# Kernel tuning notes

Hardware: AMD Instinct MI355X
Metric: run time of the kernel (lower is better)

## Reference

```python
import jax, jax.numpy as jnp
import numpy as np

B, SQ, SK = 2, 2048, 2048
D, H = 1024, 16
HD = D // H              # head_dim = 64
R = 128                  # rel_pos_max_distance
P = 2 * R + 1            # num_pos_ids = 257
RADIUS = 256             # local_attention_radius


def setup_inputs() -> dict:
    key = jax.random.key(0)
    ks = jax.random.split(key, 8)
    s = 0.02
    return {
        "Q": jax.random.normal(ks[0], (B, SQ, D), dtype=jnp.float32),
        "K": jax.random.normal(ks[1], (B, SK, D), dtype=jnp.float32),
        "V": jax.random.normal(ks[2], (B, SK, D), dtype=jnp.float32),
        "Wq": jax.random.normal(ks[3], (D, D), dtype=jnp.float32) * s,
        "Wk": jax.random.normal(ks[4], (D, D), dtype=jnp.float32) * s,
        "Wv": jax.random.normal(ks[5], (D, D), dtype=jnp.float32) * s,
        "Wo": jax.random.normal(ks[6], (D, D), dtype=jnp.float32) * s,
        "E": jax.random.normal(ks[7], (P, D), dtype=jnp.float32) * s,  # rel_embeds
    }


def _split_heads(x, W):
    # bias-free projection then split: B x S x D -> B x H x S x HD
    y = x @ W.T
    b, s, _ = y.shape
    return y.reshape(b, s, H, HD).transpose(0, 2, 1, 3)


def reference(Q, K, V, Wq, Wk, Wv, Wo, E):
    q = _split_heads(Q, Wq)  # B,H,Sq,HD
    k = _split_heads(K, Wk)  # B,H,Sk,HD
    v = _split_heads(V, Wv)  # B,H,Sk,HD

    # rel_embeds reshape matches torch: E[p] viewed as (head_dim, num_heads)
    rel = E.reshape(P, HD, H).transpose(2, 0, 1)           # H,P,HD
    Q_rel = jnp.einsum("bhqd,hpd->bhqp", q, rel)           # B,H,Sq,P

    # slided relative position ids: clip(j - i, -R, R) + R
    i = jnp.arange(SQ)[:, None]
    j = jnp.arange(SK)[None, :]
    rel_ids = jnp.clip(j - i, -R, R) + R                   # Sq,Sk
    rel_shift = jnp.take_along_axis(
        Q_rel, jnp.broadcast_to(rel_ids, (B, H, SQ, SK)), axis=3
    )                                                       # B,H,Sq,Sk

    energy = (jnp.einsum("bhqd,bhkd->bhqk", q, k) + rel_shift) / jnp.sqrt(
        jnp.float32(HD)
    )

    # local attention mask: True = masked (outside window of radius RADIUS)
    mask = jnp.abs(j - i) > RADIUS                          # Sq,Sk
    mask = mask & ~jnp.all(mask, axis=-1, keepdims=True)    # never mask full rows
    energy = jnp.where(mask[None, None], -jnp.inf, energy)

    attn = jax.nn.softmax(energy, axis=-1)                  # B,H,Sq,Sk
    out = jnp.einsum("bhqk,bhkd->bhqd", attn, v)            # B,H,Sq,HD
    # torch: view(B,H,Sq,HD).permute(0,2,3,1).flatten(2,3) -> B,Sq,(HD*H)
    out = out.transpose(0, 2, 3, 1).reshape(B, SQ, D)
    return out @ Wo.T
```

## Files before the change

### kernel.cpp

```cpp
#include <hip/hip_runtime.h>
#include <hip/hip_bf16.h>

#define BATCH 2
#define SQn 2048
#define SKn 2048
#define DMODEL 1024
#define NH 16
#define HD 64
#define NPOS 257
#define RWIN 128
#define RADIUS 256

typedef __attribute__((ext_vector_type(8))) short bf16x8;
typedef __attribute__((ext_vector_type(4))) float f32x4;

static __device__ __forceinline__ unsigned short f2bf(float f) {
    union { float f; unsigned u; } v; v.f = f;
    unsigned r = (v.u + 0x7FFFu + ((v.u >> 16) & 1u)) >> 16;
    return (unsigned short)r;
}
static __device__ __forceinline__ float bf2f(unsigned short b) {
    union { unsigned u; float f; } v; v.u = ((unsigned)b) << 16;
    return v.f;
}

static __device__ __forceinline__ void gl_lds16(const unsigned short* g, unsigned short* l) {
    __builtin_amdgcn_global_load_lds(
        (const __attribute__((address_space(1))) unsigned*)g,
        (__attribute__((address_space(3))) unsigned*)l, 16, 0, 0);
}

#define SWZ(row) (((row) ^ ((row) >> 2)) & 3)

__global__ __launch_bounds__(256) void convert_kernel(
    const float* __restrict__ Q, const float* __restrict__ K, const float* __restrict__ V,
    const float* __restrict__ Wq, const float* __restrict__ Wk, const float* __restrict__ Wv,
    const float* __restrict__ Wo,
    unsigned short* __restrict__ xb,
    unsigned short* __restrict__ wb,
    unsigned short* __restrict__ woh)
{
    int i = blockIdx.x * 256 + threadIdx.x;
    if (i < 3145728) {
        int which = i >> 20;
        int off = i & 1048575;
        const float* src = which == 0 ? Q : (which == 1 ? K : V);
        unsigned short* dst = xb + (size_t)which * 4194304;
        float4 v4 = ((const float4*)src)[off];
        ushort4 o4;
        o4.x = f2bf(v4.x); o4.y = f2bf(v4.y); o4.z = f2bf(v4.z); o4.w = f2bf(v4.w);
        ((ushort4*)dst)[off] = o4;
    } else {
        int i2 = i - 3145728;
        int which = i2 >> 18;
        int off = i2 & 262143;
        if (which < 3) {
            const float* src = which == 0 ? Wq : (which == 1 ? Wk : Wv);
            unsigned short* dst = wb + (size_t)which * 1048576;
            float4 v4 = ((const float4*)src)[off];
            ushort4 o4;
            o4.x = f2bf(v4.x); o4.y = f2bf(v4.y); o4.z = f2bf(v4.z); o4.w = f2bf(v4.w);
            ((ushort4*)dst)[off] = o4;
        } else {
            float4 v4 = ((const float4*)Wo)[off];
            int e0 = off * 4;
            int n  = e0 >> 10;
            int c0 = e0 & 1023;
            int d  = c0 >> 4;
            int h0 = c0 & 15;
            woh[((size_t)(h0 + 0) * 1024 + n) * 64 + d] = f2bf(v4.x);
            woh[((size_t)(h0 + 1) * 1024 + n) * 64 + d] = f2bf(v4.y);
            woh[((size_t)(h0 + 2) * 1024 + n) * 64 + d] = f2bf(v4.z);
            woh[((size_t)(h0 + 3) * 1024 + n) * 64 + d] = f2bf(v4.w);
        }
    }
}

__global__ __launch_bounds__(256) void mfma_gemm(
    const unsigned short* __restrict__ Xall,
    const unsigned short* __restrict__ Wall,
    unsigned short* __restrict__ Yall)
{
    __shared__ unsigned short sA[128 * 64];
    __shared__ unsigned short sB[128 * 64];
    __shared__ unsigned short sT[64 * 136];

    const int tid  = threadIdx.x;
    const int wv   = tid >> 6;
    const int lane = tid & 63;
    const int quad = lane >> 4;
    const int l15  = lane & 15;
    const int z    = blockIdx.z;
    const int m0   = blockIdx.x * 128;
    const int n0   = blockIdx.y * 128;
    const int wr   = (wv >> 1) * 64;
    const int wc   = (wv & 1) * 64;

    const unsigned short* X = Xall + (size_t)z * (4096 * 1024);
    const unsigned short* W = Wall + (size_t)z * (1024 * 1024);

    int srow[4], scc[4];
#pragma unroll
    for (int it = 0; it < 4; ++it) {
        int f = it * 256 + tid;
        srow[it] = f >> 3;
        scc[it]  = ((f & 7) ^ (srow[it] & 7)) * 8;
    }

    int aoff[2][4], boff[2][4];
#pragma unroll
    for (int ks = 0; ks < 2; ++ks)
#pragma unroll
        for (int t = 0; t < 4; ++t) {
            int R = wr + t * 16 + l15;
            aoff[ks][t] = R * 64 + ((((ks << 2) + quad) ^ (R & 7)) * 8);
            int C = wc + t * 16 + l15;
            boff[ks][t] = C * 64 + ((((ks << 2) + quad) ^ (C & 7)) * 8);
        }

    f32x4 acc[4][4];
#pragma unroll
    for (int i = 0; i < 4; ++i)
#pragma unroll
        for (int j = 0; j < 4; ++j)
            acc[i][j] = (f32x4){0.f, 0.f, 0.f, 0.f};

#pragma unroll
    for (int it = 0; it < 4; ++it) {
        gl_lds16(X + (size_t)(m0 + srow[it]) * 1024 + scc[it], &sA[(it * 256 + tid) * 8]);
        gl_lds16(W + (size_t)(n0 + srow[it]) * 1024 + scc[it], &sB[(it * 256 + tid) * 8]);
    }

    for (int k0 = 0; k0 < 1024; k0 += 64) {
        __syncthreads();

        bf16x8 a0[4], b0[4];
#pragma unroll
        for (int t = 0; t < 4; ++t) a0[t] = *(const bf16x8*)&sA[aoff[0][t]];
#pragma unroll
        for (int t = 0; t < 4; ++t) b0[t] = *(const bf16x8*)&sB[boff[0][t]];
#pragma unroll
        for (int i = 0; i < 4; ++i)
#pragma unroll
            for (int j = 0; j < 4; ++j)
                acc[i][j] = __builtin_amdgcn_mfma_f32_16x16x32_bf16(a0[i], b0[j], acc[i][j], 0, 0, 0);

        bf16x8 a1[4], b1[4];
#pragma unroll
        for (int t = 0; t < 4; ++t) a1[t] = *(const bf16x8*)&sA[aoff[1][t]];
#pragma unroll
        for (int t = 0; t < 4; ++t) b1[t] = *(const bf16x8*)&sB[boff[1][t]];
        __syncthreads();

        if (k0 + 64 < 1024) {
            const int kn = k0 + 64;
#pragma unroll
            for (int it = 0; it < 4; ++it) {
                gl_lds16(X + (size_t)(m0 + srow[it]) * 1024 + kn + scc[it], &sA[(it * 256 + tid) * 8]);
                gl_lds16(W + (size_t)(n0 + srow[it]) * 1024 + kn + scc[it], &sB[(it * 256 + tid) * 8]);
            }
        }
#pragma unroll
        for (int i = 0; i < 4; ++i)
#pragma unroll
            for (int j = 0; j < 4; ++j)
                acc[i][j] = __builtin_amdgcn_mfma_f32_16x16x32_bf16(a1[i], b1[j], acc[i][j], 0, 0, 0);
    }

    unsigned short* Y = Yall + (size_t)z * (4096 * 1024);
    const int b_ = m0 >> 11;
    const int s0 = m0 & (SQn - 1);

    if (z < 2) {
#pragma unroll
        for (int i = 0; i < 4; ++i) {
            int mbase = s0 + wr + i * 16 + quad * 4;
#pragma unroll
            for (int j = 0; j < 4; ++j) {
                int col = n0 + wc + j * 16 + l15;
                int h = col >> 6, dd = col & 63;
                unsigned short* yb = Y + (((size_t)(b_ * NH + h) * SQn) << 6) + dd;
#pragma unroll
                for (int r = 0; r < 4; ++r)
                    yb[(size_t)(mbase + r) << 6] = f2bf(acc[i][j][r]);
            }
        }
    } else {
#pragma unroll
        for (int hh = 0; hh < 2; ++hh) {
            __syncthreads();
            if ((wv & 1) == hh) {
#pragma unroll
                for (int i = 0; i < 4; ++i) {
                    int mloc = wr + i * 16 + quad * 4;
#pragma unroll
                    for (int j = 0; j < 4; ++j) {
                        ushort4 pk;
                        pk.x = f2bf(acc[i][j][0]);
                        pk.y = f2bf(acc[i][j][1]);
                        pk.z = f2bf(acc[i][j][2]);
                        pk.w = f2bf(acc[i][j][3]);
                        *(ushort4*)&sT[(j * 16 + l15) * 136 + mloc] = pk;
                    }
                }
            }
            __syncthreads();
            int h = (n0 >> 6) + hh;
            unsigned short* yb = Y + ((size_t)(b_ * NH + h) * HD) * SKn + s0;
#pragma unroll
            for (int it = 0; it < 4; ++it) {
                int u = it * 256 + tid;
                int dd = u >> 4, mc = u & 15;
                uint4 val = *(const uint4*)&sT[dd * 136 + mc * 8];
                *(uint4*)(yb + (size_t)dd * SKn + mc * 8) = val;
            }
        }
    }
}

__global__ __launch_bounds__(256) void gemm_out(
    const unsigned short* __restrict__ aoh,
    const unsigned short* __restrict__ woh,
    float* __restrict__ Y)
{
    __shared__ unsigned short sA[64 * 64];
    __shared__ unsigned short sB[128 * 64];

    const int tid  = threadIdx.x;
    const int wv   = tid >> 6;
    const int lane = tid & 63;
    const int quad = lane >> 4;
    const int l15  = lane & 15;
    const int m0   = blockIdx.x * 64;
    const int n0   = blockIdx.y * 128;
    const int wr   = (wv >> 1) * 32;
    const int wc   = (wv & 1) * 64;
    const int b_   = m0 >> 11;
    const int s0   = m0 & (SQn - 1);

    int rowa[2], ca[2];
#pragma unroll
    for (int it = 0; it < 2; ++it) {
        int f = it * 256 + tid;
        rowa[it] = f >> 3;
        ca[it]   = ((f & 7) ^ (rowa[it] & 7)) * 8;
    }
    int rowb[4], cb[4];
#pragma unroll
    for (int it = 0; it < 4; ++it) {
        int f = it * 256 + tid;
        rowb[it] = f >> 3;
        cb[it]   = ((f & 7) ^ (rowb[it] & 7)) * 8;
    }

    int aoff[2][2], boff[2][4];
#pragma unroll
    for (int ks = 0; ks < 2; ++ks) {
#pragma unroll
        for (int i = 0; i < 2; ++i) {
            int R = wr + i * 16 + l15;
            aoff[ks][i] = R * 64 + ((((ks << 2) + quad) ^ (R & 7)) * 8);
        }
#pragma unroll
        for (int j = 0; j < 4; ++j) {
            int C = wc + j * 16 + l15;
            boff[ks][j] = C * 64 + ((((ks << 2) + quad) ^ (C & 7)) * 8);
        }
    }

    f32x4 acc[2][4];
#pragma unroll
    for (int i = 0; i < 2; ++i)
#pragma unroll
        for (int j = 0; j < 4; ++j)
            acc[i][j] = (f32x4){0.f, 0.f, 0.f, 0.f};

    {
        const unsigned short* Ah = aoh + ((size_t)(b_ * NH) * SQn + s0) * HD;
        const unsigned short* Bh = woh + (size_t)n0 * HD;
#pragma unroll
        for (int it = 0; it < 2; ++it)
            gl_lds16(Ah + (size_t)rowa[it] * HD + ca[it], &sA[(it * 256 + tid) * 8]);
#pragma unroll
        for (int it = 0; it < 4; ++it)
            gl_lds16(Bh + (size_t)rowb[it] * HD + cb[it], &sB[(it * 256 + tid) * 8]);
    }

    for (int h = 0; h < NH; ++h) {
        __syncthreads();

        bf16x8 a0[2], b0[4];
#pragma unroll
        for (int i = 0; i < 2; ++i) a0[i] = *(const bf16x8*)&sA[aoff[0][i]];
#pragma unroll
        for (int j = 0; j < 4; ++j) b0[j] = *(const bf16x8*)&sB[boff[0][j]];
#pragma unroll
        for (int i = 0; i < 2; ++i)
#pragma unroll
            for (int j = 0; j < 4; ++j)
                acc[i][j] = __builtin_amdgcn_mfma_f32_16x16x32_bf16(a0[i], b0[j], acc[i][j], 0, 0, 0);

        bf16x8 a1[2], b1[4];
#pragma unroll
        for (int i = 0; i < 2; ++i) a1[i] = *(const bf16x8*)&sA[aoff[1][i]];
#pragma unroll
        for (int j = 0; j < 4; ++j) b1[j] = *(const bf16x8*)&sB[boff[1][j]];
        __syncthreads();

        if (h + 1 < NH) {
            const unsigned short* Ah = aoh + ((size_t)(b_ * NH + h + 1) * SQn + s0) * HD;
            const unsigned short* Bh = woh + ((size_t)(h + 1) * 1024 + n0) * HD;
#pragma unroll
            for (int it = 0; it < 2; ++it)
                gl_lds16(Ah + (size_t)rowa[it] * HD + ca[it], &sA[(it * 256 + tid) * 8]);
#pragma unroll
            for (int it = 0; it < 4; ++it)
                gl_lds16(Bh + (size_t)rowb[it] * HD + cb[it], &sB[(it * 256 + tid) * 8]);
        }
#pragma unroll
        for (int i = 0; i < 2; ++i)
#pragma unroll
            for (int j = 0; j < 4; ++j)
                acc[i][j] = __builtin_amdgcn_mfma_f32_16x16x32_bf16(a1[i], b1[j], acc[i][j], 0, 0, 0);
    }

#pragma unroll
    for (int i = 0; i < 2; ++i) {
        int mbase = m0 + wr + i * 16 + quad * 4;
#pragma unroll
        for (int j = 0; j < 4; ++j) {
            int col = n0 + wc + j * 16 + l15;
#pragma unroll
            for (int r = 0; r < 4; ++r)
                Y[(size_t)(mbase + r) * DMODEL + col] = acc[i][j][r];
        }
    }
}

__global__ __launch_bounds__(256) void relt_kernel(
    const float* __restrict__ E, unsigned short* __restrict__ relTb)
{
    int idx = blockIdx.x * 256 + threadIdx.x;
    const int total = NH * NPOS * HD;
    if (idx < total) {
        int d = idx & (HD - 1);
        int p = (idx >> 6) % NPOS;
        int h = idx / (NPOS * HD);
        relTb[idx] = f2bf(E[(size_t)p * DMODEL + d * NH + h]);
    }
}

#define BIAS_S2 0.0014089565402528222f
#define SC2     0.1803368801111204f

__global__ __launch_bounds__(256, 2) void attn_mfma(
    const unsigned short* __restrict__ q,
    const unsigned short* __restrict__ k,
    const unsigned short* __restrict__ vT,
    const unsigned short* __restrict__ relTb,
    unsigned short* __restrict__ aoh)
{
    __shared__ unsigned short sK[64 * 64];
    __shared__ unsigned short sVt[64 * 64];
    __shared__ unsigned short sP[4][16 * 72];
    __shared__ signed char    sq8[128 * 260];
    unsigned short* const sQ = (unsigned short*)sq8;

    const int tid  = threadIdx.x;
    const int w    = tid >> 6;
    const int lane = tid & 63;
    const int quad = lane >> 4;
    const int l15  = lane & 15;
    const int xcd  = blockIdx.x & 7;
    const int sidx = blockIdx.x >> 3;
    const int bh   = (xcd << 2) | (sidx >> 4);
    const int q0   = (sidx & 15) << 7;
    const int h    = bh & (NH - 1);

    const int f1 = tid,       row1 = f1 >> 3;
    const int c1 = ((f1 & 7) ^ (row1 & 7)) * 8;
    const int f2 = 256 + tid, row2 = f2 >> 3;
    const int c2 = ((f2 & 7) ^ (row2 & 7)) * 8;

    {
        const unsigned short* gq = q + ((size_t)bh * SQn + q0) * HD;
#pragma unroll
        for (int it = 0; it < 4; ++it) {
            int f = it * 256 + tid;
            int row = f >> 3;
            int c = ((f & 7) ^ (row & 7)) * 8;
            gl_lds16(gq + row * HD + c, &sQ[f * 8]);
        }
    }
    __syncthreads();

    const int qrow = w * 16 + l15;
    const int qs = (quad ^ (qrow & 7)) * 8;
    bf16x8 a0A = *(const bf16x8*)&sQ[qrow * 64 + qs];
    bf16x8 a1A = *(const bf16x8*)&sQ[qrow * 64 + (qs ^ 32)];
    bf16x8 a0B = *(const bf16x8*)&sQ[(64 + qrow) * 64 + qs];
    bf16x8 a1B = *(const bf16x8*)&sQ[(64 + qrow) * 64 + (qs ^ 32)];

    const int myrow = w * 16 + quad * 4;
    for (int c5 = 0; c5 < 5; ++c5) {
        __syncthreads();
        const unsigned short* gr = relTb + ((size_t)h * NPOS + c5 * 64) * HD;
        gl_lds16(gr + row1 * HD + c1, &sK[f1 * 8]);
        gl_lds16(gr + row2 * HD + c2, &sK[f2 * 8]);
        __syncthreads();
#pragma unroll
        for (int t = 0; t < 4; ++t) {
            int prow = t * 16 + l15;
            int ks = (quad ^ (prow & 7)) * 8;
            bf16x8 b0 = *(const bf16x8*)&sK[prow * 64 + ks];
            bf16x8 b1 = *(const bf16x8*)&sK[prow * 64 + (ks ^ 32)];
            f32x4 ccA = {0.f, 0.f, 0.f, 0.f};
            ccA = __builtin_amdgcn_mfma_f32_16x16x32_bf16(a0A, b0, ccA, 0, 0, 0);
            ccA = __builtin_amdgcn_mfma_f32_16x16x32_bf16(a1A, b1, ccA, 0, 0, 0);
            f32x4 ccB = {0.f, 0.f, 0.f, 0.f};
            ccB = __builtin_amdgcn_mfma_f32_16x16x32_bf16(a0B, b0, ccB, 0, 0, 0);
            ccB = __builtin_amdgcn_mfma_f32_16x16x32_bf16(a1B, b1, ccB, 0, 0, 0);
            int pos = c5 * 64 + t * 16 + l15;
            if (pos < NPOS) {
#pragma unroll
                for (int r = 0; r < 4; ++r) {
                    int iqA = (int)rintf(ccA[r] * 128.0f);
                    iqA = iqA < -127 ? -127 : (iqA > 127 ? 127 : iqA);
                    sq8[(myrow + r) * 260 + pos] = (signed char)iqA;
                    int iqB = (int)rintf(ccB[r] * 128.0f);
                    iqB = iqB < -127 ? -127 : (iqB > 127 ? 127 : iqB);
                    sq8[(64 + myrow + r) * 260 + pos] = (signed char)iqB;
                }
            }
        }
    }
    __syncthreads();

    float bias0A[4], bias256A[4], bias0B[4], bias256B[4];
#pragma unroll
    for (int r = 0; r < 4; ++r) {
        bias0A[r]   = (float)sq8[(myrow + r) * 260 + 0]          * BIAS_S2;
        bias256A[r] = (float)sq8[(myrow + r) * 260 + 256]        * BIAS_S2;
        bias0B[r]   = (float)sq8[(64 + myrow + r) * 260 + 0]     * BIAS_S2;
        bias256B[r] = (float)sq8[(64 + myrow + r) * 260 + 256]   * BIAS_S2;
    }

    const int lo = (q0 - RADIUS) > 0 ? (q0 - RADIUS) : 0;
    const int hi = (q0 + 127 + RADIUS) < (SKn - 1) ? (q0 + 127 + RADIUS) : (SKn - 1);
    const int nt = ((hi - lo) >> 6) + 1;
    const int e_ = l15 - quad * 4;

    const unsigned short* kg = k  + (size_t)bh * SKn * HD;
    const unsigned short* vg = vT + (size_t)bh * HD * SKn;

    float laccA[4] = {0.f, 0.f, 0.f, 0.f};
    float laccB[4] = {0.f, 0.f, 0.f, 0.f};
    f32x4 oA[4], oB[4];
#pragma unroll
    for (int t = 0; t < 4; ++t) {
        oA[t] = (f32x4){0.f, 0.f, 0.f, 0.f};
        oB[t] = (f32x4){0.f, 0.f, 0.f, 0.f};
    }

    {
        gl_lds16(kg + (size_t)(lo + row1) * HD + c1, &sK[f1 * 8]);
        gl_lds16(kg + (size_t)(lo + row2) * HD + c2, &sK[f2 * 8]);
        gl_lds16(vg + (size_t)row1 * SKn + lo + c1, &sVt[f1 * 8]);
        gl_lds16(vg + (size_t)row2 * SKn + lo + c2, &sVt[f2 * 8]);
    }

    for (int kt = 0; kt < nt; ++kt) {
        const int kb = lo + (kt << 6);
        __syncthreads();

        bf16x8 kf0[4], kf1[4], vf0[4], vf1[4];
#pragma unroll
        for (int t = 0; t < 4; ++t) {
            int prow = t * 16 + l15;
            int ks = (quad ^ (prow & 7)) * 8;
            kf0[t] = *(const bf16x8*)&sK[prow * 64 + ks];
            kf1[t] = *(const bf16x8*)&sK[prow * 64 + (ks ^ 32)];
            vf0[t] = *(const bf16x8*)&sVt[prow * 64 + ks];
            vf1[t] = *(const bf16x8*)&sVt[prow * 64 + (ks ^ 32)];
        }
        __syncthreads();

        if (kt + 1 < nt) {
            const int kb2 = kb + 64;
            gl_lds16(kg + (size_t)(kb2 + row1) * HD + c1, &sK[f1 * 8]);
            gl_lds16(kg + (size_t)(kb2 + row2) * HD + c2, &sK[f2 * 8]);
            gl_lds16(vg + (size_t)row1 * SKn + kb2 + c1, &sVt[f1 * 8]);
            gl_lds16(vg + (size_t)row2 * SKn + kb2 + c2, &sVt[f2 * 8]);
        }

        const int dtbaseA = kb - q0 - w * 16;
        if (dtbaseA > -320 && dtbaseA < 272) {
#pragma unroll
            for (int t = 0; t < 4; ++t) {
                const int dt = dtbaseA + t * 16;
                const int spb = (quad * 4) * 72 + t * 16 + l15;
                if (dt <= -272 || dt >= 272) {
#pragma unroll
                    for (int r = 0; r < 4; ++r) sP[w][spb + r * 72] = 0;
                } else {
                    f32x4 sc = {0.f, 0.f, 0.f, 0.f};
                    sc = __builtin_amdgcn_mfma_f32_16x16x32_bf16(a0A, kf0[t], sc, 0, 0, 0);
                    sc = __builtin_amdgcn_mfma_f32_16x16x32_bf16(a1A, kf1[t], sc, 0, 0, 0);

                    float pv[4];
                    if (dt >= -112 && dt <= 112) {
                        int idx0 = myrow * 260 + dt + 128 + e_;
#pragma unroll
                        for (int r = 0; r < 4; ++r) {
                            float bf = (float)sq8[idx0 + r * 259] * BIAS_S2;
                            pv[r] = __builtin_amdgcn_exp2f(fmaf(sc[r], SC2, bf));
                        }
                    } else if (dt >= -240 && dt <= -144) {
#pragma unroll
                        for (int r = 0; r < 4; ++r)
                            pv[r] = __builtin_amdgcn_exp2f(fmaf(sc[r], SC2, bias0A[r]));
                    } else if (dt >= 144 && dt <= 240) {
#pragma unroll
                        for (int r = 0; r < 4; ++r)
                            pv[r] = __builtin_amdgcn_exp2f(fmaf(sc[r], SC2, bias256A[r]));
                    } else {
#pragma unroll
                        for (int r = 0; r < 4; ++r) {
                            int d = dt + e_ - r;
                            bool in = (unsigned)(d + RADIUS) <= 2u * RADIUS;
                            int p = d < -RWIN ? 0 : (d > RWIN ? 2 * RWIN : d + RWIN);
                            float bf = (float)sq8[(myrow + r) * 260 + p] * BIAS_S2;
                            float e = __builtin_amdgcn_exp2f(fmaf(sc[r], SC2, bf));
                            pv[r] = in ? e : 0.0f;
                        }
                    }
#pragma unroll
                    for (int r = 0; r < 4; ++r) {
                        unsigned short pb = f2bf(pv[r]);
                        sP[w][spb + r * 72] = pb;
                        laccA[r] += bf2f(pb);
                    }
                }
            }
            bf16x8 p0 = *(const bf16x8*)&sP[w][l15 * 72 + quad * 8];
            bf16x8 p1 = *(const bf16x8*)&sP[w][l15 * 72 + 32 + quad * 8];
#pragma unroll
            for (int t = 0; t < 4; ++t) {
                oA[t] = __builtin_amdgcn_mfma_f32_16x16x32_bf16(p0, vf0[t], oA[t], 0, 0, 0);
                oA[t] = __builtin_amdgcn_mfma_f32_16x16x32_bf16(p1, vf1[t], oA[t], 0, 0, 0);
            }
        }

        const int dtbaseB = dtbaseA - 64;
        if (dtbaseB > -320 && dtbaseB < 272) {
#pragma unroll
            for (int t = 0; t < 4; ++t) {
                const int dt = dtbaseB + t * 16;
                const int spb = (quad * 4) * 72 + t * 16 + l15;
                if (dt <= -272 || dt >= 272) {
#pragma unroll
                    for (int r = 0; r < 4; ++r) sP[w][spb + r * 72] = 0;
                } else {
                    f32x4 sc = {0.f, 0.f, 0.f, 0.f};
                    sc = __builtin_amdgcn_mfma_f32_16x16x32_bf16(a0B, kf0[t], sc, 0, 0, 0);
                    sc = __builtin_amdgcn_mfma_f32_16x16x32_bf16(a1B, kf1[t], sc, 0, 0, 0);

                    float pv[4];
                    if (dt >= -112 && dt <= 112) {
                        int idx0 = (64 + myrow) * 260 + dt + 128 + e_;
#pragma unroll
                        for (int r = 0; r < 4; ++r) {
                            float bf = (float)sq8[idx0 + r * 259] * BIAS_S2;
                            pv[r] = __builtin_amdgcn_exp2f(fmaf(sc[r], SC2, bf));
                        }
                    } else if (dt >= -240 && dt <= -144) {
#pragma unroll
                        for (int r = 0; r < 4; ++r)
                            pv[r] = __builtin_amdgcn_exp2f(fmaf(sc[r], SC2, bias0B[r]));
                    } else if (dt >= 144 && dt <= 240) {
#pragma unroll
                        for (int r = 0; r < 4; ++r)
                            pv[r] = __builtin_amdgcn_exp2f(fmaf(sc[r], SC2, bias256B[r]));
                    } else {
#pragma unroll
                        for (int r = 0; r < 4; ++r) {
                            int d = dt + e_ - r;
                            bool in = (unsigned)(d + RADIUS) <= 2u * RADIUS;
                            int p = d < -RWIN ? 0 : (d > RWIN ? 2 * RWIN : d + RWIN);
                            float bf = (float)sq8[(64 + myrow + r) * 260 + p] * BIAS_S2;
                            float e = __builtin_amdgcn_exp2f(fmaf(sc[r], SC2, bf));
                            pv[r] = in ? e : 0.0f;
                        }
                    }
#pragma unroll
                    for (int r = 0; r < 4; ++r) {
                        unsigned short pb = f2bf(pv[r]);
                        sP[w][spb + r * 72] = pb;
                        laccB[r] += bf2f(pb);
                    }
                }
            }
            bf16x8 p0 = *(const bf16x8*)&sP[w][l15 * 72 + quad * 8];
            bf16x8 p1 = *(const bf16x8*)&sP[w][l15 * 72 + 32 + quad * 8];
#pragma unroll
            for (int t = 0; t < 4; ++t) {
                oB[t] = __builtin_amdgcn_mfma_f32_16x16x32_bf16(p0, vf0[t], oB[t], 0, 0, 0);
                oB[t] = __builtin_amdgcn_mfma_f32_16x16x32_bf16(p1, vf1[t], oB[t], 0, 0, 0);
            }
        }
    }

    float linvA[4], linvB[4];
#pragma unroll
    for (int r = 0; r < 4; ++r) {
        float lA = laccA[r];
        float lB = laccB[r];
#pragma unroll
        for (int off = 1; off <= 8; off <<= 1) {
            lA += __shfl_xor(lA, off);
            lB += __shfl_xor(lB, off);
        }
        linvA[r] = 1.0f / lA;
        linvB[r] = 1.0f / lB;
    }

    unsigned short* ob = aoh + ((size_t)bh * SQn + q0) * HD;
#pragma unroll
    for (int t = 0; t < 4; ++t) {
#pragma unroll
        for (int r = 0; r < 4; ++r) {
            int irow = w * 16 + quad * 4 + r;
            ob[irow * HD + t * 16 + l15] = f2bf(oA[t][r] * linvA[r]);
            ob[(64 + irow) * HD + t * 16 + l15] = f2bf(oB[t][r] * linvB[r]);
        }
    }
}

extern "C" void kernel_launch(void* const* d_in, const int* in_sizes, int n_in,
                              void* d_out, int out_size, void* d_ws, size_t ws_size,
                              hipStream_t stream) {
    const float* Q  = (const float*)d_in[0];
    const float* K  = (const float*)d_in[1];
    const float* V  = (const float*)d_in[2];
    const float* Wq = (const float*)d_in[3];
    const float* Wk = (const float*)d_in[4];
    const float* Wv = (const float*)d_in[5];
    const float* Wo = (const float*)d_in[6];
    const float* E  = (const float*)d_in[7];
    float* out = (float*)d_out;

    char* p = (char*)d_ws;
    unsigned short* xb    = (unsigned short*)p; p += (size_t)24 << 20;
    unsigned short* wb    = (unsigned short*)p; p += (size_t)6  << 20;
    unsigned short* woh   = (unsigned short*)p; p += (size_t)2  << 20;
    unsigned short* head  = (unsigned short*)p; p += (size_t)24 << 20;
    unsigned short* relTb = (unsigned short*)p; p += (size_t)1  << 20;
    unsigned short* aoh   = (unsigned short*)p;

    unsigned short* qb  = head;
    unsigned short* kb  = head + 4194304;
    unsigned short* vTb = head + 8388608;

    dim3 bb(256);
    convert_kernel<<<dim3(16384), bb, 0, stream>>>(Q, K, V, Wq, Wk, Wv, Wo, xb, wb, woh);
    relt_kernel<<<dim3(1028), bb, 0, stream>>>(E, relTb);
    mfma_gemm<<<dim3(32, 8, 3), bb, 0, stream>>>(xb, wb, head);
    attn_mfma<<<dim3(BATCH * NH * (SQn / 128)), bb, 0, stream>>>(qb, kb, vTb, relTb, aoh);
    gemm_out<<<dim3(64, 8), bb, 0, stream>>>(aoh, woh, out);
}
```

Measured before the change: 205.0 us.

## Double-buffer LDS tiles in projection and output GEMMs

The projection GEMM moves to a K-step of 32 with two LDS buffers and a new swizzle, so the next tile's global-to-LDS load is issued before computing on the current one, with a single barrier per step. The output GEMM also gets ping-pong LDS buffers for its per-head A and B tiles and drops its second barrier. This is meant to overlap global loads with MFMA work and cut synchronisation. The cost is more LDS per block in gemm_out, which may lower occupancy, and twice as many loop iterations in the projection GEMM.

```diff
diff --git a/kernel.cpp b/kernel.cpp
--- a/kernel.cpp
+++ b/kernel.cpp
@@ -29,8 +29,6 @@
         (const __attribute__((address_space(1))) unsigned*)g,
         (__attribute__((address_space(3))) unsigned*)l, 16, 0, 0);
 }
-
-#define SWZ(row) (((row) ^ ((row) >> 2)) & 3)
 
 __global__ __launch_bounds__(256) void convert_kernel(
     const float* __restrict__ Q, const float* __restrict__ K, const float* __restrict__ V,
@@ -81,9 +79,7 @@
     const unsigned short* __restrict__ Wall,
     unsigned short* __restrict__ Yall)
 {
-    __shared__ unsigned short sA[128 * 64];
-    __shared__ unsigned short sB[128 * 64];
-    __shared__ unsigned short sT[64 * 136];
+    __shared__ unsigned short S[16384];
 
     const int tid  = threadIdx.x;
     const int wv   = tid >> 6;
@@ -99,24 +95,22 @@
     const unsigned short* X = Xall + (size_t)z * (4096 * 1024);
     const unsigned short* W = Wall + (size_t)z * (1024 * 1024);
 
-    int srow[4], scc[4];
-#pragma unroll
-    for (int it = 0; it < 4; ++it) {
+    int srow[2], scol[2];
+#pragma unroll
+    for (int it = 0; it < 2; ++it) {
         int f = it * 256 + tid;
-        srow[it] = f >> 3;
-        scc[it]  = ((f & 7) ^ (srow[it] & 7)) * 8;
-    }
-
-    int aoff[2][4], boff[2][4];
-#pragma unroll
-    for (int ks = 0; ks < 2; ++ks)
-#pragma unroll
-        for (int t = 0; t < 4; ++t) {
-            int R = wr + t * 16 + l15;
-            aoff[ks][t] = R * 64 + ((((ks << 2) + quad) ^ (R & 7)) * 8);
-            int C = wc + t * 16 + l15;
-            boff[ks][t] = C * 64 + ((((ks << 2) + quad) ^ (C & 7)) * 8);
-        }
+        srow[it] = f >> 2;
+        scol[it] = ((f & 3) ^ ((srow[it] >> 1) & 3)) * 8;
+    }
+
+    int aoff[4], boff[4];
+#pragma unroll
+    for (int t = 0; t < 4; ++t) {
+        int R = wr + t * 16 + l15;
+        aoff[t] = R * 32 + ((quad ^ ((R >> 1) & 3)) * 8);
+        int C = wc + t * 16 + l15;
+        boff[t] = C * 32 + ((quad ^ ((C >> 1) & 3)) * 8);
+    }
 
     f32x4 acc[4][4];
 #pragma unroll
@@ -126,45 +120,41 @@
             acc[i][j] = (f32x4){0.f, 0.f, 0.f, 0.f};
 
 #pragma unroll
-    for (int it = 0; it < 4; ++it) {
-        gl_lds16(X + (size_t)(m0 + srow[it]) * 1024 + scc[it], &sA[(it * 256 + tid) * 8]);
-        gl_lds16(W + (size_t)(n0 + srow[it]) * 1024 + scc[it], &sB[(it * 256 + tid) * 8]);
-    }
-
-    for (int k0 = 0; k0 < 1024; k0 += 64) {
+    for (int it = 0; it < 2; ++it) {
+        int f = it * 256 + tid;
+        gl_lds16(X + (size_t)(m0 + srow[it]) * 1024 + scol[it], &S[f * 8]);
+        gl_lds16(W + (size_t)(n0 + srow[it]) * 1024 + scol[it], &S[8192 + f * 8]);
+    }
+
+    for (int k0 = 0; k0 < 1024; k0 += 32) {
+        const int cur = (k0 >> 5) & 1;
         __syncthreads();
 
-        bf16x8 a0[4], b0[4];
-#pragma unroll
-        for (int t = 0; t < 4; ++t) a0[t] = *(const bf16x8*)&sA[aoff[0][t]];
-#pragma unroll
-        for (int t = 0; t < 4; ++t) b0[t] = *(const bf16x8*)&sB[boff[0][t]];
+        if (k0 + 32 < 1024) {
+            const int nxt = cur ^ 1;
+            const int kn = k0 + 32;
+#pragma unroll
+            for (int it = 0; it < 2; ++it) {
+                int f = it * 256 + tid;
+                gl_lds16(X + (size_t)(m0 + srow[it]) * 1024 + kn + scol[it],
+                         &S[nxt * 4096 + f * 8]);
+                gl_lds16(W + (size_t)(n0 + srow[it]) * 1024 + kn + scol[it],
+                         &S[8192 + nxt * 4096 + f * 8]);
+            }
+        }
+
+        const unsigned short* bA = &S[cur * 4096];
+        const unsigned short* bB = &S[8192 + cur * 4096];
+        bf16x8 a[4], b[4];
+#pragma unroll
+        for (int t = 0; t < 4; ++t) a[t] = *(const bf16x8*)&bA[aoff[t]];
+#pragma unroll
+        for (int t = 0; t < 4; ++t) b[t] = *(const bf16x8*)&bB[boff[t]];
 #pragma unroll
         for (int i = 0; i < 4; ++i)
 #pragma unroll
             for (int j = 0; j < 4; ++j)
-                acc[i][j] = __builtin_amdgcn_mfma_f32_16x16x32_bf16(a0[i], b0[j], acc[i][j], 0, 0, 0);
-
-        bf16x8 a1[4], b1[4];
-#pragma unroll
-        for (int t = 0; t < 4; ++t) a1[t] = *(const bf16x8*)&sA[aoff[1][t]];
-#pragma unroll
-        for (int t = 0; t < 4; ++t) b1[t] = *(const bf16x8*)&sB[boff[1][t]];
-        __syncthreads();
-
-        if (k0 + 64 < 1024) {
-            const int kn = k0 + 64;
-#pragma unroll
-            for (int it = 0; it < 4; ++it) {
-                gl_lds16(X + (size_t)(m0 + srow[it]) * 1024 + kn + scc[it], &sA[(it * 256 + tid) * 8]);
-                gl_lds16(W + (size_t)(n0 + srow[it]) * 1024 + kn + scc[it], &sB[(it * 256 + tid) * 8]);
-            }
-        }
-#pragma unroll
-        for (int i = 0; i < 4; ++i)
-#pragma unroll
-            for (int j = 0; j < 4; ++j)
-                acc[i][j] = __builtin_amdgcn_mfma_f32_16x16x32_bf16(a1[i], b1[j], acc[i][j], 0, 0, 0);
+                acc[i][j] = __builtin_amdgcn_mfma_f32_16x16x32_bf16(a[i], b[j], acc[i][j], 0, 0, 0);
     }
 
     unsigned short* Y = Yall + (size_t)z * (4096 * 1024);
@@ -186,6 +176,7 @@
             }
         }
     } else {
+        unsigned short* const sT = S;
 #pragma unroll
         for (int hh = 0; hh < 2; ++hh) {
             __syncthreads();
@@ -223,8 +214,7 @@
     const unsigned short* __restrict__ woh,
     float* __restrict__ Y)
 {
-    __shared__ unsigned short sA[64 * 64];
-    __shared__ unsigned short sB[128 * 64];
+    __shared__ unsigned short S[24576];
 
     const int tid  = threadIdx.x;
     const int wv   = tid >> 6;
@@ -280,20 +270,38 @@
         const unsigned short* Bh = woh + (size_t)n0 * HD;
 #pragma unroll
         for (int it = 0; it < 2; ++it)
-            gl_lds16(Ah + (size_t)rowa[it] * HD + ca[it], &sA[(it * 256 + tid) * 8]);
+            gl_lds16(Ah + (size_t)rowa[it] * HD + ca[it], &S[(it * 256 + tid) * 8]);
 #pragma unroll
         for (int it = 0; it < 4; ++it)
-            gl_lds16(Bh + (size_t)rowb[it] * HD + cb[it], &sB[(it * 256 + tid) * 8]);
+            gl_lds16(Bh + (size_t)rowb[it] * HD + cb[it], &S[8192 + (it * 256 + tid) * 8]);
     }
 
     for (int h = 0; h < NH; ++h) {
+        const int cur = h & 1;
         __syncthreads();
 
+        if (h + 1 < NH) {
+            const int nxt = cur ^ 1;
+            const unsigned short* Ah = aoh + ((size_t)(b_ * NH + h + 1) * SQn + s0) * HD;
+            const unsigned short* Bh = woh + ((size_t)(h + 1) * 1024 + n0) * HD;
+#pragma unroll
+            for (int it = 0; it < 2; ++it)
+                gl_lds16(Ah + (size_t)rowa[it] * HD + ca[it],
+                         &S[nxt * 4096 + (it * 256 + tid) * 8]);
+#pragma unroll
+            for (int it = 0; it < 4; ++it)
+                gl_lds16(Bh + (size_t)rowb[it] * HD + cb[it],
+                         &S[8192 + nxt * 8192 + (it * 256 + tid) * 8]);
+        }
+
+        const unsigned short* bA = &S[cur * 4096];
+        const unsigned short* bB = &S[8192 + cur * 8192];
+
         bf16x8 a0[2], b0[4];
 #pragma unroll
-        for (int i = 0; i < 2; ++i) a0[i] = *(const bf16x8*)&sA[aoff[0][i]];
-#pragma unroll
-        for (int j = 0; j < 4; ++j) b0[j] = *(const bf16x8*)&sB[boff[0][j]];
+        for (int i = 0; i < 2; ++i) a0[i] = *(const bf16x8*)&bA[aoff[0][i]];
+#pragma unroll
+        for (int j = 0; j < 4; ++j) b0[j] = *(const bf16x8*)&bB[boff[0][j]];
 #pragma unroll
         for (int i = 0; i < 2; ++i)
 #pragma unroll
@@ -302,21 +310,9 @@
 
         bf16x8 a1[2], b1[4];
 #pragma unroll
-        for (int i = 0; i < 2; ++i) a1[i] = *(const bf16x8*)&sA[aoff[1][i]];
-#pragma unroll
-        for (int j = 0; j < 4; ++j) b1[j] = *(const bf16x8*)&sB[boff[1][j]];
-        __syncthreads();
-
-        if (h + 1 < NH) {
-            const unsigned short* Ah = aoh + ((size_t)(b_ * NH + h + 1) * SQn + s0) * HD;
-            const unsigned short* Bh = woh + ((size_t)(h + 1) * 1024 + n0) * HD;
-#pragma unroll
-            for (int it = 0; it < 2; ++it)
-                gl_lds16(Ah + (size_t)rowa[it] * HD + ca[it], &sA[(it * 256 + tid) * 8]);
-#pragma unroll
-            for (int it = 0; it < 4; ++it)
-                gl_lds16(Bh + (size_t)rowb[it] * HD + cb[it], &sB[(it * 256 + tid) * 8]);
-        }
+        for (int i = 0; i < 2; ++i) a1[i] = *(const bf16x8*)&bA[aoff[1][i]];
+#pragma unroll
+        for (int j = 0; j < 4; ++j) b1[j] = *(const bf16x8*)&bB[boff[1][j]];
 #pragma unroll
         for (int i = 0; i < 2; ++i)
 #pragma unroll
```

Result: no change. 208.8 us (+1.9%).
